# Kernel optimization log

Hardware: AMD Instinct MI355X
Metric: run time of the kernel (lower is better)

## Reference

```python
import jax, jax.numpy as jnp
import numpy as np

C_IN, SEQ_LEN, N_KERNELS, KSS, KS_MAX, BATCH = 1, 512, 1000, [7, 9, 11], 11, 64


def setup_inputs() -> dict:
    rng = np.random.default_rng(0)
    ks_l, dil_l, pad_l, lout_l = [], [], [], []
    W = np.zeros((N_KERNELS, C_IN, KS_MAX), dtype=np.float32)
    for k in range(N_KERNELS):
        ks = int(rng.choice(KSS))
        d_f = 2.0 ** rng.uniform(0.0, np.log2((SEQ_LEN - 1) // (ks - 1)))
        pad = int((ks - 1) * d_f // 2) if rng.integers(2) == 1 else 0
        d = int(d_f)
        # torch passes padding=2*pad to Conv1d -> adds 2*pad on EACH side
        lout = SEQ_LEN + 4 * pad - d * (ks - 1)
        w = rng.standard_normal((1, C_IN, ks)).astype(np.float32)
        w -= w.mean()  # center like the original (global mean)
        W[k, :, :ks] = w[0]
        ks_l.append(ks); dil_l.append(d); pad_l.append(pad); lout_l.append(lout)
    dils = np.asarray(dil_l, dtype=np.int64)
    pads = np.asarray(pad_l, dtype=np.int64)
    l_out = np.asarray(lout_l, dtype=np.int32)
    max_L = int(l_out.max())
    t = np.arange(max_L)
    j = np.arange(KS_MAX)
    # raw input index for output position t, tap j of kernel k
    raw = t[None, None, :] - 2 * pads[:, None, None] + j[None, :, None] * dils[:, None, None]
    valid = (raw >= 0) & (raw < SEQ_LEN)  # zero-padding semantics
    idx = np.clip(raw, 0, SEQ_LEN - 1).astype(np.int32)
    bias = (2.0 * (rng.random(N_KERNELS) - 0.5)).astype(np.float32)
    key = jax.random.key(0)
    x = jax.random.normal(key, (BATCH, C_IN, SEQ_LEN), dtype=jnp.float32)
    return {
        "x": x,
        "weight": jnp.asarray(W),
        "bias": jnp.asarray(bias),
        "idx": jnp.asarray(idx),
        "valid": jnp.asarray(valid),
        "l_out": jnp.asarray(l_out),
    }


def _forward(x, weight, bias, idx, valid, l_out):
    B = x.shape[0]
    K, C, KS = weight.shape
    L = idx.shape[-1]
    validf = valid.astype(x.dtype)  # [K, KS, L]
    acc = jnp.zeros((B, K, L), dtype=x.dtype)
    for j in range(KS):  # fixed small tap loop; each kernel vectorized over K
        xg = x[:, :, idx[:, j, :]]  # [B, C, K, L] gather along time
        acc = acc + jnp.einsum("bckt,kc->bkt", xg, weight[:, :, j]) * validf[None, :, j, :]
    out = acc + bias[None, :, None]  # [B, K, L]
    tmask = jnp.arange(L)[None, :] < l_out[:, None]  # [K, L] valid output positions
    neg = jnp.finfo(x.dtype).min
    mx = jnp.max(jnp.where(tmask[None], out, neg), axis=-1)  # [B, K]
    ppv = jnp.sum(jnp.where(tmask[None] & (out > 0), 1.0, 0.0), axis=-1) / l_out.astype(x.dtype)[None]
    # torch interleaves [max_i, ppv_i] along dim=1
    return jnp.stack([mx, ppv], axis=-1).reshape(B, 2 * K)


def reference(x, weight, bias, idx, valid, l_out):
    return _forward(x, weight, bias, idx, valid, l_out)
```

## Files before the change

### kernel.cpp

```cpp
#include <hip/hip_runtime.h>
#include <hip/hip_fp16.h>
#include <float.h>

constexpr int KMAX  = 11;
constexpr int SEQ   = 512;
constexpr int NB    = 64;
constexpr int NBB   = 8;
constexpr int NGRP  = NB / NBB;
constexpr int MSTR  = 32;
constexpr int WSLOT = 1600;

__device__ __forceinline__ unsigned h2b(__half2 h) { unsigned u; __builtin_memcpy(&u, &h, 4); return u; }
__device__ __forceinline__ __half2  b2h(unsigned u) { __half2 h; __builtin_memcpy(&h, &u, 4); return h; }

__device__ __forceinline__ unsigned pkmax(unsigned a, unsigned b) {
    unsigned d; asm("v_pk_max_f16 %0, %1, %2" : "=v"(d) : "v"(a), "v"(b)); return d;
}
__device__ __forceinline__ unsigned pkadd(unsigned a, unsigned b) { return h2b(__hadd2(b2h(a), b2h(b))); }
__device__ __forceinline__ __half2 h2max(__half2 a, __half2 b) { return b2h(pkmax(h2b(a), h2b(b))); }
__device__ __forceinline__ unsigned pkfma_clamp(unsigned a, unsigned b, unsigned c) {
    unsigned d; asm("v_pk_fma_f16 %0, %1, %2, %3 clamp" : "=v"(d) : "v"(a), "v"(b), "v"(c)); return d;
}

template<int CTRL>
__device__ __forceinline__ unsigned dppmov(unsigned old, unsigned v) {
    return (unsigned)__builtin_amdgcn_update_dpp((int)old, (int)v, CTRL, 0xF, 0xF, false);
}
constexpr unsigned NEGINF2 = 0xFC00FC00u;

__device__ __forceinline__ unsigned dpp_redmax(unsigned x) {
    x = pkmax(x, dppmov<0xB1 >(NEGINF2, x));
    x = pkmax(x, dppmov<0x4E >(NEGINF2, x));
    x = pkmax(x, dppmov<0x141>(NEGINF2, x));
    x = pkmax(x, dppmov<0x140>(NEGINF2, x));
    x = pkmax(x, dppmov<0x142>(NEGINF2, x));
    x = pkmax(x, dppmov<0x143>(NEGINF2, x));
    return x;
}
__device__ __forceinline__ unsigned dpp_redadd(unsigned x) {
    x = pkadd(x, dppmov<0xB1 >(0u, x));
    x = pkadd(x, dppmov<0x4E >(0u, x));
    x = pkadd(x, dppmov<0x141>(0u, x));
    x = pkadd(x, dppmov<0x140>(0u, x));
    x = pkadd(x, dppmov<0x142>(0u, x));
    x = pkadd(x, dppmov<0x143>(0u, x));
    return x;
}

__global__ __launch_bounds__(256)
void prep_kernel(const float* __restrict__ x, const float* __restrict__ w,
                 const int* __restrict__ idx, int* __restrict__ meta,
                 unsigned short* __restrict__ xt, int K, int maxL)
{
    const int tid = threadIdx.x;
    if ((int)blockIdx.x >= K) {
        const int j  = ((int)blockIdx.x - K) * 256 + tid;
        const int b  = j >> 7;
        const int s4 = j & 127;
        const float4 v = reinterpret_cast<const float4*>(x)[b * (SEQ / 4) + s4];
        const int g = b >> 3, bl = b & 7;
        unsigned short* dst = xt + ((size_t)g * SEQ + s4 * 4) * NBB + bl;
        __half h;
        h = __float2half_rn(v.x); __builtin_memcpy(&dst[0 * NBB], &h, 2);
        h = __float2half_rn(v.y); __builtin_memcpy(&dst[1 * NBB], &h, 2);
        h = __float2half_rn(v.z); __builtin_memcpy(&dst[2 * NBB], &h, 2);
        h = __float2half_rn(v.w); __builtin_memcpy(&dst[3 * NBB], &h, 2);
        return;
    }

    __shared__ int c_sh[KMAX];
    const int k = blockIdx.x, wave = tid >> 6, lane = tid & 63;

    for (int j = wave; j < KMAX; j += 4) {
        const int* row = idx + ((size_t)k * KMAX + j) * (size_t)maxL;
        int c = 0;
        for (int base = 0; base < maxL; base += 64) {
            const int t = base + lane;
            const int v = (t < maxL) ? row[t] : 0;
            const bool interior = (v > 0) && (v < SEQ - 1);
            const unsigned long long mb = __ballot(interior);
            if (mb != 0ull) {
                const int fl = __builtin_ctzll(mb);
                c = __shfl(v, fl) - (base + fl);
                break;
            }
        }
        if (lane == 0) c_sh[j] = c;
    }
    __syncthreads();

    if (tid == 0) {
        int* mk = meta + (size_t)k * MSTR;
        int n = 0, cmin = 0, cmax = 0;
        for (int j = 0; j < KMAX; ++j) {
            const float wj = w[(size_t)k * KMAX + j];
            if (wj != 0.0f) {
                const int c = c_sh[j];
                mk[1 + n] = c;
                __half hw = __float2half_rn(wj);
                unsigned short ub; __builtin_memcpy(&ub, &hw, 2);
                mk[12 + n] = (unsigned)ub | ((unsigned)ub << 16);
                cmin = min(cmin, c); cmax = max(cmax, c);
                ++n;
            }
        }
        for (int jj = n; jj < KMAX; ++jj) { mk[1 + jj] = 0; mk[12 + jj] = 0; }
        mk[0]  = n;
        mk[23] = cmin;
        mk[24] = cmax;
    }
}

template<int NJ>
__device__ __forceinline__ void conv_body(
    const char* __restrict__ xsc, const int* __restrict__ msh,
    int lout, int x0, int wave, int lane, unsigned ctermb,
    __half2 (&mx2)[4], __half2 (&ct2)[4])
{
    const __half2 zero2 = __float2half2_rn(0.f);
    const __half2 nbig2 = __float2half2_rn(-65504.f);
    const unsigned C4b  = 0x74007400u;

    int addr[NJ]; __half2 wr[NJ];
#pragma unroll
    for (int j = 0; j < NJ; ++j) {
        const int c = __builtin_amdgcn_readfirstlane(msh[1 + j]);
        wr[j]   = b2h((unsigned)__builtin_amdgcn_readfirstlane(msh[12 + j]));
        addr[j] = (wave * 64 + lane + c + x0) * 16;
    }
#pragma unroll
    for (int m = 0; m < 4; ++m) { mx2[m] = nbig2; ct2[m] = zero2; }

#pragma unroll
    for (int it = 0; it < 4; ++it) {
        const int tb = wave * 64 + it * 256;
        if (tb + 64 <= lout) {
            uint4 d[NJ];
#pragma unroll
            for (int j = 0; j < NJ; ++j)
                d[j] = *reinterpret_cast<const uint4*>(xsc + addr[j] + it * 4096);
            __half2 a[4] = {zero2, zero2, zero2, zero2};
#pragma unroll
            for (int j = 0; j < NJ; ++j) {
                a[0] = __hfma2(wr[j], b2h(d[j].x), a[0]);
                a[1] = __hfma2(wr[j], b2h(d[j].y), a[1]);
                a[2] = __hfma2(wr[j], b2h(d[j].z), a[2]);
                a[3] = __hfma2(wr[j], b2h(d[j].w), a[3]);
            }
#pragma unroll
            for (int m = 0; m < 4; ++m) {
                mx2[m] = h2max(mx2[m], a[m]);
                ct2[m] = b2h(pkadd(h2b(ct2[m]), pkfma_clamp(h2b(a[m]), C4b, ctermb)));
            }
        }
    }

    const int rem = lout & 63;
    if (rem) {
        const int pc = lout >> 6;
        if ((pc & 3) == wave) {
            const int off = (pc >> 2) << 12;
            uint4 d[NJ];
#pragma unroll
            for (int j = 0; j < NJ; ++j)
                d[j] = *reinterpret_cast<const uint4*>(xsc + addr[j] + off);
            __half2 a[4] = {zero2, zero2, zero2, zero2};
#pragma unroll
            for (int j = 0; j < NJ; ++j) {
                a[0] = __hfma2(wr[j], b2h(d[j].x), a[0]);
                a[1] = __hfma2(wr[j], b2h(d[j].y), a[1]);
                a[2] = __hfma2(wr[j], b2h(d[j].z), a[2]);
                a[3] = __hfma2(wr[j], b2h(d[j].w), a[3]);
            }
            const bool tm = lane < rem;
#pragma unroll
            for (int m = 0; m < 4; ++m) {
                a[m] = tm ? a[m] : nbig2;
                mx2[m] = h2max(mx2[m], a[m]);
                ct2[m] = b2h(pkadd(h2b(ct2[m]), pkfma_clamp(h2b(a[m]), C4b, ctermb)));
            }
        }
    }
}

__global__ __launch_bounds__(256, 6)
void rocket_main(const unsigned short* __restrict__ xt, const int* __restrict__ meta,
                 const float* __restrict__ bias, const int* __restrict__ l_out,
                 float* __restrict__ out, int K)
{
    __shared__ __align__(16) unsigned xs_u[WSLOT * 4];
    __shared__ unsigned redm[4][4], redc[4][4];
    __shared__ int msh[MSTR];

    const int k    = blockIdx.x;
    const int grp  = blockIdx.y;
    const int tid  = threadIdx.x;
    const int wave = __builtin_amdgcn_readfirstlane(tid >> 6);
    const int lane = tid & 63;

    if (tid < MSTR) msh[tid] = meta[(size_t)k * MSTR + tid];
    __syncthreads();

    const int   x0    = -msh[23];
    const int   lout  = l_out[k];
    const float biasf = bias[k];
    const int   uend  = min(WSLOT, lout + 63 + msh[24] + x0 + 1);

    float4* xs4 = reinterpret_cast<float4*>(xs_u);
    const float4 z4 = make_float4(0.f, 0.f, 0.f, 0.f);
    for (int i = tid; i < x0; i += 256) xs4[i] = z4;
    for (int i = x0 + SEQ + tid; i < uend; i += 256) xs4[i] = z4;
    const float4* src = reinterpret_cast<const float4*>(xt + (size_t)grp * SEQ * NBB);
    xs4[x0 + tid]       = src[tid];
    xs4[x0 + 256 + tid] = src[256 + tid];
    __syncthreads();

    const int      nj     = __builtin_amdgcn_readfirstlane(msh[0]);
    const unsigned ctermb = h2b(__float2half2_rn(biasf * 16384.f));

    __half2 mx2[4], ct2[4];
    const char* xsc = reinterpret_cast<const char*>(xs_u);
    if (nj <= 7)      conv_body<7 >(xsc, msh, lout, x0, wave, lane, ctermb, mx2, ct2);
    else if (nj <= 9) conv_body<9 >(xsc, msh, lout, x0, wave, lane, ctermb, mx2, ct2);
    else              conv_body<11>(xsc, msh, lout, x0, wave, lane, ctermb, mx2, ct2);

    unsigned um[4], uc[4];
#pragma unroll
    for (int m = 0; m < 4; ++m) {
        um[m] = dpp_redmax(h2b(mx2[m]));
        uc[m] = dpp_redadd(h2b(ct2[m]));
    }
    if (lane == 63) {
#pragma unroll
        for (int m = 0; m < 4; ++m) { redm[wave][m] = um[m]; redc[wave][m] = uc[m]; }
    }
    __syncthreads();

    if (tid < 16) {
        const int bl = tid >> 1, kind = tid & 1;
        const int m = bl >> 1, hi = bl & 1;
        const int b = grp * NBB + bl;
        if (kind == 0) {
            float v = -FLT_MAX;
#pragma unroll
            for (int wv = 0; wv < 4; ++wv) {
                const __half2 h = b2h(redm[wv][m]);
                v = fmaxf(v, hi ? __high2float(h) : __low2float(h));
            }
            out[(size_t)b * (2 * K) + 2 * k] = v + biasf;
        } else {
            float s = 0.f;
#pragma unroll
            for (int wv = 0; wv < 4; ++wv) {
                const __half2 h = b2h(redc[wv][m]);
                s += hi ? __high2float(h) : __low2float(h);
            }
            out[(size_t)b * (2 * K) + 2 * k + 1] = s / (float)lout;
        }
    }
}

extern "C" void kernel_launch(void* const* d_in, const int* in_sizes, int n_in,
                              void* d_out, int out_size, void* d_ws, size_t ws_size,
                              hipStream_t stream)
{
    const float* x    = (const float*)d_in[0];
    const float* w    = (const float*)d_in[1];
    const float* bias = (const float*)d_in[2];
    const int*   idx  = (const int*)d_in[3];
    const int*   lout = (const int*)d_in[5];
    float* out = (float*)d_out;

    const int K    = in_sizes[2];
    const int maxL = in_sizes[3] / (K * KMAX);

    int* meta = (int*)d_ws;
    size_t meta_bytes = ((size_t)K * MSTR * sizeof(int) + 255) & ~(size_t)255;
    unsigned short* xt = (unsigned short*)((char*)d_ws + meta_bytes);

    prep_kernel<<<K + 32, 256, 0, stream>>>(x, w, idx, meta, xt, K, maxL);
    rocket_main<<<dim3(K, NGRP), 256, 0, stream>>>(xt, meta, bias, lout, out, K);
}
```

Baseline: 33.54 us.

## Shrink LDS window with fixed padding and clamped addresses to raise occupancy

Replaces the per-kernel variable-size LDS window (up to 1600 slots, with dynamic zero-fill ranges) with a fixed 640-slot window that has 64 zero slots on each side. Tap addresses are clamped to the window, so out-of-range taps read zeros. This cuts LDS use per block, allowing launch_bounds to rise from 6 to 8 blocks, and removes a barrier and the meta-dependent fill loops. The preprocessing kernel now finds each tap offset with a strided first probe and falls back to a full scan only if that probe finds nothing. Padded dummy taps get a large offset. The risk is that clamping correctness depends on the window covering every in-range tap, and the extra min/max per load adds ALU work.

```diff
diff --git a/kernel.cpp b/kernel.cpp
--- a/kernel.cpp
+++ b/kernel.cpp
@@ -8,7 +8,9 @@
 constexpr int NBB   = 8;
 constexpr int NGRP  = NB / NBB;
 constexpr int MSTR  = 32;
-constexpr int WSLOT = 1600;
+constexpr int WSLOT = 640;
+constexpr int X0    = 64;
+constexpr int WHI   = (WSLOT - 1) * 16;
 
 __device__ __forceinline__ unsigned h2b(__half2 h) { unsigned u; __builtin_memcpy(&u, &h, 4); return u; }
 __device__ __forceinline__ __half2  b2h(unsigned u) { __half2 h; __builtin_memcpy(&h, &u, 4); return h; }
@@ -73,16 +75,28 @@
 
     for (int j = wave; j < KMAX; j += 4) {
         const int* row = idx + ((size_t)k * KMAX + j) * (size_t)maxL;
-        int c = 0;
-        for (int base = 0; base < maxL; base += 64) {
-            const int t = base + lane;
-            const int v = (t < maxL) ? row[t] : 0;
+        int c = 1 << 20;
+        {
+            const int t = min(lane * 16, maxL - 1);
+            const int v = row[t];
             const bool interior = (v > 0) && (v < SEQ - 1);
             const unsigned long long mb = __ballot(interior);
             if (mb != 0ull) {
                 const int fl = __builtin_ctzll(mb);
-                c = __shfl(v, fl) - (base + fl);
-                break;
+                const int tf = min(fl * 16, maxL - 1);
+                c = __shfl(v, fl) - tf;
+            } else {
+                for (int base = 0; base < maxL; base += 64) {
+                    const int t2 = base + lane;
+                    const int v2 = (t2 < maxL) ? row[t2] : 0;
+                    const bool in2 = (v2 > 0) && (v2 < SEQ - 1);
+                    const unsigned long long mb2 = __ballot(in2);
+                    if (mb2 != 0ull) {
+                        const int fl2 = __builtin_ctzll(mb2);
+                        c = __shfl(v2, fl2) - (base + fl2);
+                        break;
+                    }
+                }
             }
         }
         if (lane == 0) c_sh[j] = c;
@@ -91,42 +105,38 @@
 
     if (tid == 0) {
         int* mk = meta + (size_t)k * MSTR;
-        int n = 0, cmin = 0, cmax = 0;
+        int n = 0;
         for (int j = 0; j < KMAX; ++j) {
             const float wj = w[(size_t)k * KMAX + j];
             if (wj != 0.0f) {
-                const int c = c_sh[j];
-                mk[1 + n] = c;
+                mk[1 + n] = c_sh[j];
                 __half hw = __float2half_rn(wj);
                 unsigned short ub; __builtin_memcpy(&ub, &hw, 2);
                 mk[12 + n] = (unsigned)ub | ((unsigned)ub << 16);
-                cmin = min(cmin, c); cmax = max(cmax, c);
                 ++n;
             }
         }
-        for (int jj = n; jj < KMAX; ++jj) { mk[1 + jj] = 0; mk[12 + jj] = 0; }
-        mk[0]  = n;
-        mk[23] = cmin;
-        mk[24] = cmax;
+        for (int jj = n; jj < KMAX; ++jj) { mk[1 + jj] = 1 << 20; mk[12 + jj] = 0; }
+        mk[0] = n;
     }
 }
 
 template<int NJ>
 __device__ __forceinline__ void conv_body(
     const char* __restrict__ xsc, const int* __restrict__ msh,
-    int lout, int x0, int wave, int lane, unsigned ctermb,
+    int lout, int wave, int lane, unsigned ctermb,
     __half2 (&mx2)[4], __half2 (&ct2)[4])
 {
     const __half2 zero2 = __float2half2_rn(0.f);
     const __half2 nbig2 = __float2half2_rn(-65504.f);
     const unsigned C4b  = 0x74007400u;
 
-    int addr[NJ]; __half2 wr[NJ];
+    int sb[NJ]; __half2 wr[NJ];
 #pragma unroll
     for (int j = 0; j < NJ; ++j) {
         const int c = __builtin_amdgcn_readfirstlane(msh[1 + j]);
-        wr[j]   = b2h((unsigned)__builtin_amdgcn_readfirstlane(msh[12 + j]));
-        addr[j] = (wave * 64 + lane + c + x0) * 16;
+        wr[j] = b2h((unsigned)__builtin_amdgcn_readfirstlane(msh[12 + j]));
+        sb[j] = (wave * 64 + lane + X0 + c) * 16;
     }
 #pragma unroll
     for (int m = 0; m < 4; ++m) { mx2[m] = nbig2; ct2[m] = zero2; }
@@ -137,20 +147,22 @@
         if (tb + 64 <= lout) {
             uint4 d[NJ];
 #pragma unroll
-            for (int j = 0; j < NJ; ++j)
-                d[j] = *reinterpret_cast<const uint4*>(xsc + addr[j] + it * 4096);
-            __half2 a[4] = {zero2, zero2, zero2, zero2};
-#pragma unroll
-            for (int j = 0; j < NJ; ++j) {
-                a[0] = __hfma2(wr[j], b2h(d[j].x), a[0]);
-                a[1] = __hfma2(wr[j], b2h(d[j].y), a[1]);
-                a[2] = __hfma2(wr[j], b2h(d[j].z), a[2]);
-                a[3] = __hfma2(wr[j], b2h(d[j].w), a[3]);
+            for (int j = 0; j < NJ; ++j) {
+                const int a = min(max(sb[j] + it * 4096, 0), WHI);
+                d[j] = *reinterpret_cast<const uint4*>(xsc + a);
+            }
+            __half2 a4[4] = {zero2, zero2, zero2, zero2};
+#pragma unroll
+            for (int j = 0; j < NJ; ++j) {
+                a4[0] = __hfma2(wr[j], b2h(d[j].x), a4[0]);
+                a4[1] = __hfma2(wr[j], b2h(d[j].y), a4[1]);
+                a4[2] = __hfma2(wr[j], b2h(d[j].z), a4[2]);
+                a4[3] = __hfma2(wr[j], b2h(d[j].w), a4[3]);
             }
 #pragma unroll
             for (int m = 0; m < 4; ++m) {
-                mx2[m] = h2max(mx2[m], a[m]);
-                ct2[m] = b2h(pkadd(h2b(ct2[m]), pkfma_clamp(h2b(a[m]), C4b, ctermb)));
+                mx2[m] = h2max(mx2[m], a4[m]);
+                ct2[m] = b2h(pkadd(h2b(ct2[m]), pkfma_clamp(h2b(a4[m]), C4b, ctermb)));
             }
         }
     }
@@ -162,28 +174,30 @@
             const int off = (pc >> 2) << 12;
             uint4 d[NJ];
 #pragma unroll
-            for (int j = 0; j < NJ; ++j)
-                d[j] = *reinterpret_cast<const uint4*>(xsc + addr[j] + off);
-            __half2 a[4] = {zero2, zero2, zero2, zero2};
-#pragma unroll
-            for (int j = 0; j < NJ; ++j) {
-                a[0] = __hfma2(wr[j], b2h(d[j].x), a[0]);
-                a[1] = __hfma2(wr[j], b2h(d[j].y), a[1]);
-                a[2] = __hfma2(wr[j], b2h(d[j].z), a[2]);
-                a[3] = __hfma2(wr[j], b2h(d[j].w), a[3]);
+            for (int j = 0; j < NJ; ++j) {
+                const int a = min(max(sb[j] + off, 0), WHI);
+                d[j] = *reinterpret_cast<const uint4*>(xsc + a);
+            }
+            __half2 a4[4] = {zero2, zero2, zero2, zero2};
+#pragma unroll
+            for (int j = 0; j < NJ; ++j) {
+                a4[0] = __hfma2(wr[j], b2h(d[j].x), a4[0]);
+                a4[1] = __hfma2(wr[j], b2h(d[j].y), a4[1]);
+                a4[2] = __hfma2(wr[j], b2h(d[j].z), a4[2]);
+                a4[3] = __hfma2(wr[j], b2h(d[j].w), a4[3]);
             }
             const bool tm = lane < rem;
 #pragma unroll
             for (int m = 0; m < 4; ++m) {
-                a[m] = tm ? a[m] : nbig2;
-                mx2[m] = h2max(mx2[m], a[m]);
-                ct2[m] = b2h(pkadd(h2b(ct2[m]), pkfma_clamp(h2b(a[m]), C4b, ctermb)));
-            }
-        }
-    }
-}
-
-__global__ __launch_bounds__(256, 6)
+                a4[m] = tm ? a4[m] : nbig2;
+                mx2[m] = h2max(mx2[m], a4[m]);
+                ct2[m] = b2h(pkadd(h2b(ct2[m]), pkfma_clamp(h2b(a4[m]), C4b, ctermb)));
+            }
+        }
+    }
+}
+
+__global__ __launch_bounds__(256, 8)
 void rocket_main(const unsigned short* __restrict__ xt, const int* __restrict__ meta,
                  const float* __restrict__ bias, const int* __restrict__ l_out,
                  float* __restrict__ out, int K)
@@ -199,30 +213,27 @@
     const int lane = tid & 63;
 
     if (tid < MSTR) msh[tid] = meta[(size_t)k * MSTR + tid];
+
+    float4* xs4 = reinterpret_cast<float4*>(xs_u);
+    if (tid < 2 * X0) {
+        const int slot = (tid < X0) ? tid : tid + SEQ;
+        xs4[slot] = make_float4(0.f, 0.f, 0.f, 0.f);
+    }
+    const float4* src = reinterpret_cast<const float4*>(xt + (size_t)grp * SEQ * NBB);
+    xs4[X0 + tid]       = src[tid];
+    xs4[X0 + 256 + tid] = src[256 + tid];
     __syncthreads();
 
-    const int   x0    = -msh[23];
-    const int   lout  = l_out[k];
-    const float biasf = bias[k];
-    const int   uend  = min(WSLOT, lout + 63 + msh[24] + x0 + 1);
-
-    float4* xs4 = reinterpret_cast<float4*>(xs_u);
-    const float4 z4 = make_float4(0.f, 0.f, 0.f, 0.f);
-    for (int i = tid; i < x0; i += 256) xs4[i] = z4;
-    for (int i = x0 + SEQ + tid; i < uend; i += 256) xs4[i] = z4;
-    const float4* src = reinterpret_cast<const float4*>(xt + (size_t)grp * SEQ * NBB);
-    xs4[x0 + tid]       = src[tid];
-    xs4[x0 + 256 + tid] = src[256 + tid];
-    __syncthreads();
-
     const int      nj     = __builtin_amdgcn_readfirstlane(msh[0]);
+    const int      lout   = l_out[k];
+    const float    biasf  = bias[k];
     const unsigned ctermb = h2b(__float2half2_rn(biasf * 16384.f));
 
     __half2 mx2[4], ct2[4];
     const char* xsc = reinterpret_cast<const char*>(xs_u);
-    if (nj <= 7)      conv_body<7 >(xsc, msh, lout, x0, wave, lane, ctermb, mx2, ct2);
-    else if (nj <= 9) conv_body<9 >(xsc, msh, lout, x0, wave, lane, ctermb, mx2, ct2);
-    else              conv_body<11>(xsc, msh, lout, x0, wave, lane, ctermb, mx2, ct2);
+    if (nj <= 7)      conv_body<7 >(xsc, msh, lout, wave, lane, ctermb, mx2, ct2);
+    else if (nj <= 9) conv_body<9 >(xsc, msh, lout, wave, lane, ctermb, mx2, ct2);
+    else              conv_body<11>(xsc, msh, lout, wave, lane, ctermb, mx2, ct2);
 
     unsigned um[4], uc[4];
 #pragma unroll
```

After: 39.22 us. +16.9%, slower.
